# Performance work log

Hardware: AMD Instinct MI355X
Metric: run time of the kernel (lower is better)

The kernel has to match this reference:

```python
import jax, jax.numpy as jnp
import numpy as np


def setup_inputs() -> dict:
    key = jax.random.key(0)
    ks = jax.random.split(key, 8)
    B, C, H, W = 4, 256, 64, 64
    Ci = C // 8  # inter_channels = 32
    x = jax.random.normal(ks[0], (B, C, H, W), dtype=jnp.float32)
    # 1x1 conv weights stored as [out, in] matrices (kernel size 1)
    sq = 1.0 / np.sqrt(C)
    Wq = jax.random.uniform(ks[1], (Ci, C), jnp.float32, -sq, sq)
    bq = jax.random.uniform(ks[2], (Ci,), jnp.float32, -sq, sq)
    Wk = jax.random.uniform(ks[3], (Ci, C), jnp.float32, -sq, sq)
    bk = jax.random.uniform(ks[4], (Ci,), jnp.float32, -sq, sq)
    Wv = jax.random.uniform(ks[5], (C, C), jnp.float32, -sq, sq)
    bv = jax.random.uniform(ks[6], (C,), jnp.float32, -sq, sq)
    # torch initializes gamma to zeros; use a nonzero value so output depends on attention path
    gamma = jnp.array([0.5], dtype=jnp.float32)
    return {"x": x, "Wq": Wq, "bq": bq, "Wk": Wk, "bk": bk, "Wv": Wv, "bv": bv, "gamma": gamma}


def reference(x, Wq, bq, Wk, bk, Wv, bv, gamma):
    B, C, H, W = x.shape
    N = H * W
    xf = x.reshape(B, C, N)                        # [B, C, N]
    # 1x1 convs == channel-mixing matmuls
    q = jnp.einsum('oc,bcn->bon', Wq, xf) + bq[None, :, None]   # [B, Ci, N]
    k = jnp.einsum('oc,bcn->bon', Wk, xf) + bk[None, :, None]   # [B, Ci, N]
    v = jnp.einsum('oc,bcn->bon', Wv, xf) + bv[None, :, None]   # [B, C,  N]
    # energy[b, n, m] = sum_c q[b, c, n] * k[b, c, m]  (no scaling, per DANet)
    energy = jnp.einsum('bcn,bcm->bnm', q, k)      # [B, N, N]
    attention = jax.nn.softmax(energy, axis=-1)    # softmax over keys m
    # out[b, c, n] = sum_m v[b, c, m] * attention[b, n, m]
    out = jnp.einsum('bcm,bnm->bcn', v, attention)
    out = out.reshape(B, C, H, W)
    return gamma[0] * out + x
```

## Files before the change

### kernel.cpp

```cpp
#include <hip/hip_runtime.h>
#include <hip/hip_bf16.h>
#include <math.h>

typedef __bf16 bf16x8 __attribute__((ext_vector_type(8)));
typedef float  floatx4 __attribute__((ext_vector_type(4)));
typedef float  floatx16 __attribute__((ext_vector_type(16)));
typedef unsigned u32x2 __attribute__((ext_vector_type(2)));

#define MFMA(a, b, c)   __builtin_amdgcn_mfma_f32_16x16x32_bf16((a), (b), (c), 0, 0, 0)
#define MFMA32(a, b, c) __builtin_amdgcn_mfma_f32_32x32x16_bf16((a), (b), (c), 0, 0, 0)

__device__ __forceinline__ unsigned short f2bf(float f) {
  union { float f; unsigned u; } v; v.f = f;
  unsigned r = v.u + 0x7FFFu + ((v.u >> 16) & 1u);
  return (unsigned short)(r >> 16);
}
__device__ __forceinline__ float bf2f(unsigned short u) {
  union { unsigned u; float f; } v; v.u = ((unsigned)u) << 16;
  return v.f;
}
__device__ __forceinline__ unsigned pack2(float a, float b) {
  __bf16 x = (__bf16)a, y = (__bf16)b;
  unsigned short ux = __builtin_bit_cast(unsigned short, x);
  unsigned short uy = __builtin_bit_cast(unsigned short, y);
  return (unsigned)ux | ((unsigned)uy << 16);
}
__device__ __forceinline__ float exp2_fast(float x) {
#if __has_builtin(__builtin_amdgcn_exp2f)
  return __builtin_amdgcn_exp2f(x);
#else
  return exp2f(x);
#endif
}

__global__ __launch_bounds__(256) void k_wconv(const float* __restrict__ Wq,
                                               const float* __restrict__ Wk,
                                               const float* __restrict__ Wv,
                                               unsigned short* __restrict__ Wall) {
  int i = blockIdx.x * 256 + threadIdx.x;
  int o = i >> 8, c = i & 255;
  float v = (o < 32) ? Wq[o * 256 + c]
          : (o < 64) ? Wk[(o - 32) * 256 + c]
                     : Wv[(o - 64) * 256 + c];
  Wall[i] = f2bf(v);
}

__global__ __launch_bounds__(256) void k_xpose(const float* __restrict__ x,
                                               unsigned short* __restrict__ xT) {
  int bid = blockIdx.x;
  int b = bid >> 8, rem = bid & 255;
  int nb = rem >> 2, cb = rem & 3;
  int n0 = nb * 64, c0 = cb * 64;
  int tid = threadIdx.x;
  __shared__ alignas(16) unsigned short T[64][72];
#pragma unroll
  for (int i = 0; i < 4; ++i) {
    int idx = tid + 256 * i;
    int r = idx >> 4, g = idx & 15;
    float4 d = *(const float4*)(x + ((size_t)b * 256 + c0 + r) * 4096 + n0 + g * 4);
    T[g * 4 + 0][r] = f2bf(d.x);
    T[g * 4 + 1][r] = f2bf(d.y);
    T[g * 4 + 2][r] = f2bf(d.z);
    T[g * 4 + 3][r] = f2bf(d.w);
  }
  __syncthreads();
#pragma unroll
  for (int i = 0; i < 2; ++i) {
    int idx = tid + 256 * i;
    int j = idx >> 3, g = idx & 7;
    *(uint4*)(xT + ((size_t)b * 4096 + n0 + j) * 256 + c0 + g * 8) =
        *(const uint4*)&T[j][g * 8];
  }
}

__global__ __launch_bounds__(64, 4) void k_proj(const unsigned short* __restrict__ xT,
                                                const unsigned short* __restrict__ Wall,
                                                const float* __restrict__ bq,
                                                const float* __restrict__ bk,
                                                const float* __restrict__ bv,
                                                unsigned short* __restrict__ qbf,
                                                unsigned short* __restrict__ kbf,
                                                unsigned short* __restrict__ vbf) {
  int b = blockIdx.x >> 9;
  int m0 = ((blockIdx.x >> 1) & 255) * 16;
  int h = blockIdx.x & 1;
  int lane = threadIdx.x & 63;
  int l15 = lane & 15, quad = lane >> 4;

  floatx4 acc[10];
#pragma unroll
  for (int tt = 0; tt < 10; ++tt) acc[tt] = floatx4{0.f, 0.f, 0.f, 0.f};

  const unsigned short* arow = xT + ((size_t)b * 4096 + m0 + l15) * 256;
#pragma unroll
  for (int ks = 0; ks < 8; ++ks) {
    bf16x8 a = *(const bf16x8*)(arow + ks * 32 + quad * 8);
#pragma unroll
    for (int tt = 0; tt < 10; ++tt) {
      int gt = (tt < 2) ? (h * 2 + tt) : (4 + h * 8 + (tt - 2));
      bf16x8 w = *(const bf16x8*)(Wall + (size_t)(gt * 16 + l15) * 256 + ks * 32 + quad * 8);
      acc[tt] = MFMA(a, w, acc[tt]);
    }
  }
#pragma unroll
  for (int tt = 0; tt < 2; ++tt) {
    int o = (h * 2 + tt) * 16 + l15;
    float bias = (o < 32) ? bq[o] : bk[o - 32];
    float scale = (o < 32) ? 1.44269504088896340736f : 1.0f;
    unsigned short* dst = (o < 32) ? qbf : kbf;
    int oc = o & 31;
    int kh = oc >> 4, h2 = (oc >> 3) & 1, c8 = oc & 7;
#pragma unroll
    for (int r = 0; r < 4; ++r) {
      int m = m0 + quad * 4 + r;
      dst[(size_t)b * 131072 + (size_t)(m >> 5) * 1024 + kh * 512 + h2 * 256 +
          (m & 31) * 8 + c8] = f2bf((acc[tt][r] + bias) * scale);
    }
  }
  __shared__ alignas(16) unsigned short Os[128][24];
#pragma unroll
  for (int tt = 2; tt < 10; ++tt) {
    int lr = (tt - 2) * 16 + l15;
    int c = h * 128 + lr;
    float bias = bv[c];
#pragma unroll
    for (int r = 0; r < 4; ++r)
      Os[lr][quad * 4 + r] = f2bf(acc[tt][r] + bias);
  }
  __syncthreads();
  {
    int kb = m0 >> 5, kk = (m0 >> 4) & 1;
#pragma unroll
    for (int i = 0; i < 4; ++i) {
      int idx = threadIdx.x + 64 * i;
      int cbl = idx >> 6;
      int rem = idx & 63;
      int h2 = rem >> 5, ch = rem & 31;
      int r = cbl * 32 + ch;
      *(uint4*)(vbf + (size_t)b * 1048576 + (size_t)kb * 8192 +
                (size_t)(h * 4 + cbl) * 1024 + kk * 512 + h2 * 256 + ch * 8) =
          *(const uint4*)&Os[r][h2 * 8];
    }
  }
}

__device__ __forceinline__ void softmax_pack(floatx16 st, float& lp, bf16x8 (&pa)[2], int hi) {
  float p[16];
#pragma unroll
  for (int r = 0; r < 16; ++r) p[r] = exp2_fast(st[r]);
  lp += (((p[0] + p[1]) + (p[2] + p[3])) + ((p[4] + p[5]) + (p[6] + p[7]))) +
        (((p[8] + p[9]) + (p[10] + p[11])) + ((p[12] + p[13]) + (p[14] + p[15])));
  unsigned d0[4], d1[4];
#pragma unroll
  for (int t = 0; t < 4; ++t) {
    d0[t] = pack2(p[4 * t + 0], p[4 * t + 1]);
    d1[t] = pack2(p[4 * t + 2], p[4 * t + 3]);
  }
#pragma unroll
  for (int ks = 0; ks < 2; ++ks) {
#if __has_builtin(__builtin_amdgcn_permlane32_swap)
    (void)hi;
    u32x2 r0 = __builtin_amdgcn_permlane32_swap(d0[2 * ks], d0[2 * ks + 1], false, false);
    u32x2 r1 = __builtin_amdgcn_permlane32_swap(d1[2 * ks], d1[2 * ks + 1], false, false);
    union { unsigned u[4]; bf16x8 v; } u;
    u.u[0] = r0[0]; u.u[1] = r1[0]; u.u[2] = r0[1]; u.u[3] = r1[1];
    pa[ks] = u.v;
#else
    unsigned s0 = hi ? d0[2 * ks] : d0[2 * ks + 1];
    unsigned s1 = hi ? d1[2 * ks] : d1[2 * ks + 1];
    unsigned o0 = (unsigned)__shfl_xor((int)s0, 32);
    unsigned o1 = (unsigned)__shfl_xor((int)s1, 32);
    union { unsigned u[4]; bf16x8 v; } u;
    u.u[0] = hi ? o0 : d0[2 * ks];
    u.u[1] = hi ? o1 : d1[2 * ks];
    u.u[2] = hi ? d0[2 * ks + 1] : o0;
    u.u[3] = hi ? d1[2 * ks + 1] : o1;
    pa[ks] = u.v;
#endif
  }
}

__global__ __launch_bounds__(64, 2) void k_attn(const unsigned short* __restrict__ qbf,
                                                const unsigned short* __restrict__ kbf,
                                                const unsigned short* __restrict__ vbf,
                                                unsigned short* __restrict__ Obf,
                                                float* __restrict__ lsum) {
  int wg = (blockIdx.x & 7) * 256 + (blockIdx.x >> 3);
  const int qb = wg & 63;
  const int g  = wg >> 6;
  const int cw = g & 1;
  const int s  = (g >> 1) & 3;
  const int b  = g >> 3;
  const int lane = threadIdx.x & 63;
  const int l31 = lane & 31;
  const int hi  = lane >> 5;
  const int q0  = qb * 64;

  const floatx16 z16 = {0.f, 0.f, 0.f, 0.f, 0.f, 0.f, 0.f, 0.f,
                        0.f, 0.f, 0.f, 0.f, 0.f, 0.f, 0.f, 0.f};

  bf16x8 qf[2][2];
  {
    const unsigned short* qbase =
        qbf + (size_t)b * 131072 + (size_t)(qb * 2) * 1024 + hi * 256 + l31 * 8;
#pragma unroll
    for (int qs2 = 0; qs2 < 2; ++qs2)
#pragma unroll
      for (int kh = 0; kh < 2; ++kh)
        qf[qs2][kh] = *(const bf16x8*)(qbase + qs2 * 1024 + kh * 512);
  }

  floatx16 acc[2][4];
#pragma unroll
  for (int i = 0; i < 2; ++i)
#pragma unroll
    for (int j = 0; j < 4; ++j) acc[i][j] = z16;

  float lp0 = 0.f, lp1 = 0.f;

  const unsigned short* krow =
      kbf + (size_t)b * 131072 + (size_t)(s * 32) * 1024 + hi * 256 + l31 * 8;
  const unsigned short* vrow =
      vbf + (size_t)b * 1048576 + (size_t)(s * 32) * 8192 + (size_t)(cw * 4) * 1024 +
      hi * 256 + l31 * 8;

  bf16x8 kf0 = *(const bf16x8*)krow;
  bf16x8 kf1 = *(const bf16x8*)(krow + 512);

  for (int it = 0; it < 32; ++it) {
    bf16x8 vb[4][2];
    const unsigned short* vit = vrow + (size_t)it * 8192;
#pragma unroll
    for (int ct = 0; ct < 4; ++ct) {
      vb[ct][0] = *(const bf16x8*)(vit + ct * 1024);
      vb[ct][1] = *(const bf16x8*)(vit + ct * 1024 + 512);
    }
    const unsigned short* kn = krow + (size_t)((it + 1) & 31) * 1024;
    bf16x8 kn0 = *(const bf16x8*)kn;
    bf16x8 kn1 = *(const bf16x8*)(kn + 512);

    floatx16 st0 = MFMA32(kf0, qf[0][0], z16);
    st0 = MFMA32(kf1, qf[0][1], st0);
    floatx16 st1 = MFMA32(kf0, qf[1][0], z16);
    st1 = MFMA32(kf1, qf[1][1], st1);
    kf0 = kn0; kf1 = kn1;

    bf16x8 pa[2][2];
    softmax_pack(st0, lp0, pa[0], hi);
    softmax_pack(st1, lp1, pa[1], hi);

    __builtin_amdgcn_s_setprio(1);
#pragma unroll
    for (int ct = 0; ct < 4; ++ct) {
      acc[0][ct] = MFMA32(pa[0][0], vb[ct][0], acc[0][ct]);
      acc[1][ct] = MFMA32(pa[1][0], vb[ct][0], acc[1][ct]);
      acc[0][ct] = MFMA32(pa[0][1], vb[ct][1], acc[0][ct]);
      acc[1][ct] = MFMA32(pa[1][1], vb[ct][1], acc[1][ct]);
    }
    __builtin_amdgcn_s_setprio(0);
  }

  lp0 += __shfl_xor(lp0, 32);
  lp1 += __shfl_xor(lp1, 32);
  if (cw == 0) {
    float lv = hi ? lp1 : lp0;
    lsum[((size_t)s * 4 + b) * 4096 + q0 + hi * 32 + l31] = lv;
  }
#pragma unroll
  for (int qs2 = 0; qs2 < 2; ++qs2)
#pragma unroll
    for (int ct = 0; ct < 4; ++ct) {
      unsigned short* orow = Obf +
          (((size_t)s * 4 + b) * 256 + cw * 128 + ct * 32 + l31) * 4096 +
          q0 + qs2 * 32 + hi * 4;
#pragma unroll
      for (int gi = 0; gi < 4; ++gi) {
        unsigned w0 = pack2(acc[qs2][ct][4 * gi + 0], acc[qs2][ct][4 * gi + 1]);
        unsigned w1 = pack2(acc[qs2][ct][4 * gi + 2], acc[qs2][ct][4 * gi + 3]);
        unsigned long long w = (unsigned long long)w0 | ((unsigned long long)w1 << 32);
        *(unsigned long long*)(orow + 8 * gi) = w;
      }
    }
}

__global__ __launch_bounds__(256) void k_merge(const unsigned short* __restrict__ Obf,
                                               const float* __restrict__ lsum,
                                               const float* __restrict__ x,
                                               const float* __restrict__ gma,
                                               float* __restrict__ out) {
  int t = blockIdx.x * 256 + threadIdx.x;
  int n4 = t & 1023;
  int c = (t >> 10) & 255;
  int b = t >> 18;
  int n = n4 << 2;
  size_t xa = (((size_t)b * 256 + c) << 12) + n;
  float4 xv = *(const float4*)(x + xa);
  float L0 = 0.f, L1 = 0.f, L2 = 0.f, L3 = 0.f;
  float o0 = 0.f, o1 = 0.f, o2 = 0.f, o3 = 0.f;
#pragma unroll
  for (int s = 0; s < 4; ++s) {
    float4 ls = *(const float4*)(lsum + (((size_t)s * 4 + b) << 12) + n);
    L0 += ls.x; L1 += ls.y; L2 += ls.z; L3 += ls.w;
    ushort4 ov = *(const ushort4*)(Obf + ((((size_t)s * 4 + b) * 256 + c) << 12) + n);
    o0 += bf2f(ov.x); o1 += bf2f(ov.y); o2 += bf2f(ov.z); o3 += bf2f(ov.w);
  }
  float g = gma[0];
  float4 r;
  r.x = xv.x + g * o0 / L0;
  r.y = xv.y + g * o1 / L1;
  r.z = xv.z + g * o2 / L2;
  r.w = xv.w + g * o3 / L3;
  *(float4*)(out + xa) = r;
}

extern "C" void kernel_launch(void* const* d_in, const int* in_sizes, int n_in,
                              void* d_out, int out_size, void* d_ws, size_t ws_size,
                              hipStream_t stream) {
  const float* x   = (const float*)d_in[0];
  const float* Wq  = (const float*)d_in[1];
  const float* bq  = (const float*)d_in[2];
  const float* Wk  = (const float*)d_in[3];
  const float* bk  = (const float*)d_in[4];
  const float* Wv  = (const float*)d_in[5];
  const float* bv  = (const float*)d_in[6];
  const float* gma = (const float*)d_in[7];
  float* out = (float*)d_out;

  unsigned short* qbf  = (unsigned short*)d_ws;
  unsigned short* kbf  = qbf + (size_t)4 * 131072;
  unsigned short* vbf  = kbf + (size_t)4 * 131072;
  unsigned short* Wall = vbf + (size_t)4 * 1048576;
  unsigned short* xT   = Wall + (size_t)320 * 256;
  unsigned short* Obf  = xT;
  float* lsum = (float*)(Obf + (size_t)4 * 4 * 256 * 4096);

  k_wconv<<<320, 256, 0, stream>>>(Wq, Wk, Wv, Wall);
  k_xpose<<<1024, 256, 0, stream>>>(x, xT);
  k_proj<<<2048, 64, 0, stream>>>(xT, Wall, bq, bk, bv, qbf, kbf, vbf);
  k_attn<<<2048, 64, 0, stream>>>(qbf, kbf, vbf, Obf, lsum);
  k_merge<<<4096, 256, 0, stream>>>(Obf, lsum, x, gma, out);
}
```

Baseline: 170.5 us.

## Halve per-wave work in projection and attention kernels to double grid size

The attention kernel now handles 32 queries per wave instead of 64. Its grid doubles to 4096 waves, and launch bounds are raised to 4 waves per SIMD for higher occupancy. The projection kernel is likewise split four ways per 16-row tile instead of two, so each wave computes 5 output tiles instead of 10. The aim is more latency hiding and parallelism. In exchange, each K/V fragment loaded is reused by half as many MFMAs, which doubles K/V global traffic in the attention loop.

```diff
diff --git a/kernel.cpp b/kernel.cpp
--- a/kernel.cpp
+++ b/kernel.cpp
@@ -81,30 +81,34 @@
                                                 unsigned short* __restrict__ qbf,
                                                 unsigned short* __restrict__ kbf,
                                                 unsigned short* __restrict__ vbf) {
-  int b = blockIdx.x >> 9;
-  int m0 = ((blockIdx.x >> 1) & 255) * 16;
-  int h = blockIdx.x & 1;
+  int b = blockIdx.x >> 10;
+  int rem = blockIdx.x & 1023;
+  int m0 = (rem >> 2) * 16;
+  int qr = rem & 3;
   int lane = threadIdx.x & 63;
   int l15 = lane & 15, quad = lane >> 4;
 
-  floatx4 acc[10];
-#pragma unroll
-  for (int tt = 0; tt < 10; ++tt) acc[tt] = floatx4{0.f, 0.f, 0.f, 0.f};
+  floatx4 acc[5];
+#pragma unroll
+  for (int tt = 0; tt < 5; ++tt) acc[tt] = floatx4{0.f, 0.f, 0.f, 0.f};
 
   const unsigned short* arow = xT + ((size_t)b * 4096 + m0 + l15) * 256;
 #pragma unroll
   for (int ks = 0; ks < 8; ++ks) {
     bf16x8 a = *(const bf16x8*)(arow + ks * 32 + quad * 8);
-#pragma unroll
-    for (int tt = 0; tt < 10; ++tt) {
-      int gt = (tt < 2) ? (h * 2 + tt) : (4 + h * 8 + (tt - 2));
+    {
+      bf16x8 w = *(const bf16x8*)(Wall + (size_t)(qr * 16 + l15) * 256 + ks * 32 + quad * 8);
+      acc[0] = MFMA(a, w, acc[0]);
+    }
+#pragma unroll
+    for (int t = 0; t < 4; ++t) {
+      int gt = 4 + qr * 4 + t;
       bf16x8 w = *(const bf16x8*)(Wall + (size_t)(gt * 16 + l15) * 256 + ks * 32 + quad * 8);
-      acc[tt] = MFMA(a, w, acc[tt]);
-    }
-  }
-#pragma unroll
-  for (int tt = 0; tt < 2; ++tt) {
-    int o = (h * 2 + tt) * 16 + l15;
+      acc[1 + t] = MFMA(a, w, acc[1 + t]);
+    }
+  }
+  {
+    int o = qr * 16 + l15;
     float bias = (o < 32) ? bq[o] : bk[o - 32];
     float scale = (o < 32) ? 1.44269504088896340736f : 1.0f;
     unsigned short* dst = (o < 32) ? qbf : kbf;
@@ -114,32 +118,31 @@
     for (int r = 0; r < 4; ++r) {
       int m = m0 + quad * 4 + r;
       dst[(size_t)b * 131072 + (size_t)(m >> 5) * 1024 + kh * 512 + h2 * 256 +
-          (m & 31) * 8 + c8] = f2bf((acc[tt][r] + bias) * scale);
-    }
-  }
-  __shared__ alignas(16) unsigned short Os[128][24];
-#pragma unroll
-  for (int tt = 2; tt < 10; ++tt) {
-    int lr = (tt - 2) * 16 + l15;
-    int c = h * 128 + lr;
+          (m & 31) * 8 + c8] = f2bf((acc[0][r] + bias) * scale);
+    }
+  }
+  __shared__ alignas(16) unsigned short Os[64][24];
+#pragma unroll
+  for (int t = 0; t < 4; ++t) {
+    int lr = t * 16 + l15;
+    int c = qr * 64 + lr;
     float bias = bv[c];
 #pragma unroll
     for (int r = 0; r < 4; ++r)
-      Os[lr][quad * 4 + r] = f2bf(acc[tt][r] + bias);
+      Os[lr][quad * 4 + r] = f2bf(acc[1 + t][r] + bias);
   }
   __syncthreads();
   {
     int kb = m0 >> 5, kk = (m0 >> 4) & 1;
 #pragma unroll
-    for (int i = 0; i < 4; ++i) {
+    for (int i = 0; i < 2; ++i) {
       int idx = threadIdx.x + 64 * i;
-      int cbl = idx >> 6;
-      int rem = idx & 63;
-      int h2 = rem >> 5, ch = rem & 31;
-      int r = cbl * 32 + ch;
+      int r = idx >> 1, g = idx & 1;
+      int c = qr * 64 + r;
+      int cb = c >> 5, ch = c & 31;
       *(uint4*)(vbf + (size_t)b * 1048576 + (size_t)kb * 8192 +
-                (size_t)(h * 4 + cbl) * 1024 + kk * 512 + h2 * 256 + ch * 8) =
-          *(const uint4*)&Os[r][h2 * 8];
+                (size_t)cb * 1024 + kk * 512 + g * 256 + ch * 8) =
+          *(const uint4*)&Os[r][g * 8];
     }
   }
 }
@@ -180,43 +183,38 @@
   }
 }
 
-__global__ __launch_bounds__(64, 2) void k_attn(const unsigned short* __restrict__ qbf,
+__global__ __launch_bounds__(64, 4) void k_attn(const unsigned short* __restrict__ qbf,
                                                 const unsigned short* __restrict__ kbf,
                                                 const unsigned short* __restrict__ vbf,
                                                 unsigned short* __restrict__ Obf,
                                                 float* __restrict__ lsum) {
-  int wg = (blockIdx.x & 7) * 256 + (blockIdx.x >> 3);
-  const int qb = wg & 63;
-  const int g  = wg >> 6;
+  int wg = (blockIdx.x & 7) * 512 + (blockIdx.x >> 3);
+  const int qb = wg & 127;
+  const int g  = wg >> 7;
   const int cw = g & 1;
   const int s  = (g >> 1) & 3;
   const int b  = g >> 3;
   const int lane = threadIdx.x & 63;
   const int l31 = lane & 31;
   const int hi  = lane >> 5;
-  const int q0  = qb * 64;
+  const int q0  = qb * 32;
 
   const floatx16 z16 = {0.f, 0.f, 0.f, 0.f, 0.f, 0.f, 0.f, 0.f,
                         0.f, 0.f, 0.f, 0.f, 0.f, 0.f, 0.f, 0.f};
 
-  bf16x8 qf[2][2];
+  bf16x8 qf[2];
   {
     const unsigned short* qbase =
-        qbf + (size_t)b * 131072 + (size_t)(qb * 2) * 1024 + hi * 256 + l31 * 8;
-#pragma unroll
-    for (int qs2 = 0; qs2 < 2; ++qs2)
-#pragma unroll
-      for (int kh = 0; kh < 2; ++kh)
-        qf[qs2][kh] = *(const bf16x8*)(qbase + qs2 * 1024 + kh * 512);
-  }
-
-  floatx16 acc[2][4];
-#pragma unroll
-  for (int i = 0; i < 2; ++i)
-#pragma unroll
-    for (int j = 0; j < 4; ++j) acc[i][j] = z16;
-
-  float lp0 = 0.f, lp1 = 0.f;
+        qbf + (size_t)b * 131072 + (size_t)qb * 1024 + hi * 256 + l31 * 8;
+    qf[0] = *(const bf16x8*)(qbase);
+    qf[1] = *(const bf16x8*)(qbase + 512);
+  }
+
+  floatx16 acc[4];
+#pragma unroll
+  for (int j = 0; j < 4; ++j) acc[j] = z16;
+
+  float lp0 = 0.f;
 
   const unsigned short* krow =
       kbf + (size_t)b * 131072 + (size_t)(s * 32) * 1024 + hi * 256 + l31 * 8;
@@ -235,52 +233,43 @@
       vb[ct][0] = *(const bf16x8*)(vit + ct * 1024);
       vb[ct][1] = *(const bf16x8*)(vit + ct * 1024 + 512);
     }
+
+    floatx16 st0 = MFMA32(kf0, qf[0], z16);
+    st0 = MFMA32(kf1, qf[1], st0);
+
     const unsigned short* kn = krow + (size_t)((it + 1) & 31) * 1024;
-    bf16x8 kn0 = *(const bf16x8*)kn;
-    bf16x8 kn1 = *(const bf16x8*)(kn + 512);
-
-    floatx16 st0 = MFMA32(kf0, qf[0][0], z16);
-    st0 = MFMA32(kf1, qf[0][1], st0);
-    floatx16 st1 = MFMA32(kf0, qf[1][0], z16);
-    st1 = MFMA32(kf1, qf[1][1], st1);
-    kf0 = kn0; kf1 = kn1;
-
-    bf16x8 pa[2][2];
-    softmax_pack(st0, lp0, pa[0], hi);
-    softmax_pack(st1, lp1, pa[1], hi);
+    kf0 = *(const bf16x8*)kn;
+    kf1 = *(const bf16x8*)(kn + 512);
+
+    bf16x8 pa[2];
+    softmax_pack(st0, lp0, pa, hi);
 
     __builtin_amdgcn_s_setprio(1);
 #pragma unroll
     for (int ct = 0; ct < 4; ++ct) {
-      acc[0][ct] = MFMA32(pa[0][0], vb[ct][0], acc[0][ct]);
-      acc[1][ct] = MFMA32(pa[1][0], vb[ct][0], acc[1][ct]);
-      acc[0][ct] = MFMA32(pa[0][1], vb[ct][1], acc[0][ct]);
-      acc[1][ct] = MFMA32(pa[1][1], vb[ct][1], acc[1][ct]);
+      acc[ct] = MFMA32(pa[0], vb[ct][0], acc[ct]);
+      acc[ct] = MFMA32(pa[1], vb[ct][1], acc[ct]);
     }
     __builtin_amdgcn_s_setprio(0);
   }
 
   lp0 += __shfl_xor(lp0, 32);
-  lp1 += __shfl_xor(lp1, 32);
-  if (cw == 0) {
-    float lv = hi ? lp1 : lp0;
-    lsum[((size_t)s * 4 + b) * 4096 + q0 + hi * 32 + l31] = lv;
-  }
-#pragma unroll
-  for (int qs2 = 0; qs2 < 2; ++qs2)
-#pragma unroll
-    for (int ct = 0; ct < 4; ++ct) {
-      unsigned short* orow = Obf +
-          (((size_t)s * 4 + b) * 256 + cw * 128 + ct * 32 + l31) * 4096 +
-          q0 + qs2 * 32 + hi * 4;
-#pragma unroll
-      for (int gi = 0; gi < 4; ++gi) {
-        unsigned w0 = pack2(acc[qs2][ct][4 * gi + 0], acc[qs2][ct][4 * gi + 1]);
-        unsigned w1 = pack2(acc[qs2][ct][4 * gi + 2], acc[qs2][ct][4 * gi + 3]);
-        unsigned long long w = (unsigned long long)w0 | ((unsigned long long)w1 << 32);
-        *(unsigned long long*)(orow + 8 * gi) = w;
-      }
-    }
+  if (cw == 0 && hi == 0) {
+    lsum[((size_t)s * 4 + b) * 4096 + q0 + l31] = lp0;
+  }
+#pragma unroll
+  for (int ct = 0; ct < 4; ++ct) {
+    unsigned short* orow = Obf +
+        (((size_t)s * 4 + b) * 256 + cw * 128 + ct * 32 + l31) * 4096 +
+        q0 + hi * 4;
+#pragma unroll
+    for (int gi = 0; gi < 4; ++gi) {
+      unsigned w0 = pack2(acc[ct][4 * gi + 0], acc[ct][4 * gi + 1]);
+      unsigned w1 = pack2(acc[ct][4 * gi + 2], acc[ct][4 * gi + 3]);
+      unsigned long long w = (unsigned long long)w0 | ((unsigned long long)w1 << 32);
+      *(unsigned long long*)(orow + 8 * gi) = w;
+    }
+  }
 }
 
 __global__ __launch_bounds__(256) void k_merge(const unsigned short* __restrict__ Obf,
@@ -336,7 +325,7 @@
 
   k_wconv<<<320, 256, 0, stream>>>(Wq, Wk, Wv, Wall);
   k_xpose<<<1024, 256, 0, stream>>>(x, xT);
-  k_proj<<<2048, 64, 0, stream>>>(xT, Wall, bq, bk, bv, qbf, kbf, vbf);
-  k_attn<<<2048, 64, 0, stream>>>(qbf, kbf, vbf, Obf, lsum);
+  k_proj<<<4096, 64, 0, stream>>>(xT, Wall, bq, bk, bv, qbf, kbf, vbf);
+  k_attn<<<4096, 64, 0, stream>>>(qbf, kbf, vbf, Obf, lsum);
   k_merge<<<4096, 256, 0, stream>>>(Obf, lsum, x, gma, out);
 }
```

New measurement: 281.6 us. 1.65x slower.
